# Kernel tuning notes

Measured on AMD Instinct MI355X. Metric: run time of the kernel, lower is better.

Reference implementation:

```python
import jax, jax.numpy as jnp
import numpy as np

V, N, H, A_DIM, F_OUT = 3, 8192, 128, 64, 128


def setup_inputs() -> dict:
    key = jax.random.key(0)
    ks = jax.random.split(key, 13)
    s = 0.02
    w = lambda k, shape: jax.random.normal(k, shape, jnp.float32) * s
    adj = jax.random.randint(ks[0], (V, N, N), 0, 2, dtype=jnp.int32)
    return {
        "adjacency_matrices_list": adj,
        "W1": w(ks[1], (V, N, H)), "b1": w(ks[2], (V, H)),
        "W2": w(ks[3], (V, H, H)), "b2": w(ks[4], (V, H)),
        "Wa1": w(ks[5], (H, A_DIM)), "ba1": w(ks[6], (A_DIM,)),
        "Wa2": w(ks[7], (A_DIM, 1)), "ba2": w(ks[8], (1,)),
        "Wf1": w(ks[9], (H * V, 2 * H)), "bf1": w(ks[10], (2 * H,)),
        "Wf2": w(ks[11], (2 * H, F_OUT)), "bf2": w(ks[12], (F_OUT,)),
    }


def _norm_adj(adj_int):
    # PyG GCNConv gcn_norm on binary edges: add remaining self-loops, then D^-1/2 (A+I) D^-1/2
    a = (adj_int != 0).astype(jnp.float32)            # (V,N,N) binary
    eye = jnp.eye(adj_int.shape[-1], dtype=jnp.float32)
    ah = a * (1.0 - eye) + eye                        # force diagonal to exactly 1
    dinv = jax.lax.rsqrt(ah.sum(-1))                  # deg >= 1, safe
    return ah * dinv[..., :, None] * dinv[..., None, :]


def _forward(adj, W1, b1, W2, b2, Wa1, ba1, Wa2, ba2, Wf1, bf1, Wf2, bf2):
    A = _norm_adj(adj)                                # (V,N,N)
    # initial features X = eye(N), so A @ (X @ W1) == A @ W1
    h = jax.nn.relu(jnp.einsum('vnm,vmh->vnh', A, W1) + b1[:, None, :])
    h = jnp.einsum('vnh,vhk->vnk', h, W2)
    h = jax.nn.relu(jnp.einsum('vnm,vmk->vnk', A, h) + b2[:, None, :])  # (V,N,H) view embeddings
    # attention fusion
    summ = h.mean(axis=1)                             # (V,H) view summaries
    scores = (jnp.tanh(summ @ Wa1 + ba1) @ Wa2 + ba2)[:, 0]
    attn = jax.nn.softmax(scores, axis=0)             # (V,)
    weighted = h * attn[:, None, None]
    fusion_in = jnp.transpose(weighted, (1, 0, 2)).reshape(h.shape[1], -1)  # (N, V*H)
    fused = jax.nn.relu(fusion_in @ Wf1 + bf1) @ Wf2 + bf2                  # (N, F_OUT)
    return fused, attn, h


def reference(adjacency_matrices_list, W1, b1, W2, b2, Wa1, ba1, Wa2, ba2, Wf1, bf1, Wf2, bf2):
    return _forward(adjacency_matrices_list, W1, b1, W2, b2, Wa1, ba1, Wa2, ba2, Wf1, bf1, Wf2, bf2)
```

## Files before the change

kernel.cpp:

```cpp
#include <hip/hip_runtime.h>
#include <hip/hip_bf16.h>

#define VV 3
#define NN 8192
#define HH 128
#define ADIM 64
#define FOUT 128
#define KSPLIT 4

typedef short bf16x8 __attribute__((ext_vector_type(8)));
typedef float f32x4 __attribute__((ext_vector_type(4)));
typedef unsigned char uchar;

__device__ __forceinline__ float bf2f(ushort u) {
    union { unsigned int i; float f; } x; x.i = ((unsigned int)u) << 16; return x.f;
}
__device__ __forceinline__ ushort f2bf(float f) {
    union { float f; unsigned int i; } x; x.f = f;
    unsigned int r = (x.i + 0x7FFFu + ((x.i >> 16) & 1u)) >> 16;
    return (ushort)r;
}
__device__ __forceinline__ void async_cp16(const void* g, void* l) {
    __builtin_amdgcn_global_load_lds(
        (const __attribute__((address_space(1))) void*)g,
        (__attribute__((address_space(3))) void*)l, 16, 0, 0);
}

__global__ void zero_k(float* p, int n) {
    int i = blockIdx.x * blockDim.x + threadIdx.x;
    if (i < n) p[i] = 0.0f;
}

__global__ __launch_bounds__(256) void pack_k(const int* __restrict__ adj,
                                              uchar* __restrict__ abits,
                                              int* __restrict__ deg) {
    __shared__ uint lw[32 * 256];
    const int t = threadIdx.x;
    const int r = t >> 1, half = t & 1;
    const int ks = blockIdx.x, mt = blockIdx.y, z = blockIdx.z;
    const int m0 = mt * 128;
    const int n = m0 + r;
    const long rowoff = ((long)z * NN + n) * NN;
    int cnt = 0;
    for (int kc = 0; kc < 32; kc++) {
        const int colbase = ks * (NN / KSPLIT) + kc * 64 + half * 32;
        uint wbits = 0;
        #pragma unroll
        for (int i = 0; i < 8; i++) {
            const int c0 = colbase + i * 4;
            const int4 v = *(const int4*)(adj + rowoff + c0);
            uint b0 = (v.x != 0 || c0 + 0 == n) ? 1u : 0u;
            uint b1 = (v.y != 0 || c0 + 1 == n) ? 1u : 0u;
            uint b2 = (v.z != 0 || c0 + 2 == n) ? 1u : 0u;
            uint b3 = (v.w != 0 || c0 + 3 == n) ? 1u : 0u;
            wbits |= (b0 | (b1 << 1) | (b2 << 2) | (b3 << 3)) << (i * 4);
        }
        cnt += __popc(wbits);
        lw[kc * 256 + r * 2 + half] = wbits;
    }
    atomicAdd(&deg[z * NN + n], cnt);
    __syncthreads();
    const uint4* src = (const uint4*)lw;
    uint4* dst = (uint4*)(abits + ((((long)z * 64 + mt) * 128 + ks * 32) << 10));
    #pragma unroll
    for (int it = 0; it < 8; it++) dst[it * 256 + t] = src[it * 256 + t];
}

__global__ void dinv_k(const int* __restrict__ deg, float* __restrict__ dinv) {
    int i = blockIdx.x * blockDim.x + threadIdx.x;
    if (i < VV * NN) dinv[i] = rsqrtf((float)deg[i]);
}

template<int INF32>
__global__ void transpose_scale_k(const void* __restrict__ in_, ushort* __restrict__ out,
                                  int R, int C, const float* __restrict__ scale, int scale_z) {
    __shared__ ushort tile[32][33];
    const long zo = (long)blockIdx.z * R * C;
    const int c0 = blockIdx.x * 32, r0 = blockIdx.y * 32;
    const int t = threadIdx.x;
    #pragma unroll
    for (int p = 0; p < 4; p++) {
        int e = p * 256 + t; int row = e >> 5, col = e & 31;
        long idx = zo + (long)(r0 + row) * C + c0 + col;
        float x = INF32 ? ((const float*)in_)[idx] : bf2f(((const ushort*)in_)[idx]);
        if (scale) x *= scale[(long)blockIdx.z * scale_z + r0 + row];
        tile[row][col] = f2bf(x);
    }
    __syncthreads();
    #pragma unroll
    for (int p = 0; p < 4; p++) {
        int e = p * 256 + t; int row = e >> 5, col = e & 31;
        out[zo + (long)(c0 + row) * R + r0 + col] = tile[col][row];
    }
}

__global__ __launch_bounds__(256) void gemm_adj_k(
    const uchar* __restrict__ abits,
    const ushort* __restrict__ Bt,
    float* __restrict__ Cpart)
{
    __shared__ __align__(16) uchar As[1024];
    __shared__ __align__(16) ushort Bs[128 * 64];
    const int tid = threadIdx.x, lane = tid & 63, w = tid >> 6;
    const int wr = w >> 1, wc = w & 1;
    const int ks = blockIdx.x, mt = blockIdx.y, z = blockIdx.z;
    const int m0 = mt * 128;
    const int kbeg = ks * (NN / KSPLIT);
    const uchar* Atile = abits + (((long)z * 64 + mt) * 128 << 10);
    const ushort* Bv = Bt + (long)z * 128 * NN;
    f32x4 acc[4][4] = {};

    int srow[4], slcb[4];
    #pragma unroll
    for (int p = 0; p < 4; p++) {
        int slot = (w * 4 + p) * 64 + lane;
        srow[p] = slot >> 3;
        slcb[p] = (slot & 7) ^ (srow[p] & 7);
    }

    for (int k0 = kbeg; k0 < kbeg + NN / KSPLIT; k0 += 64) {
        if (w == 0)
            async_cp16(Atile + ((long)(k0 >> 6) << 10) + lane * 16, As + lane * 16);
        #pragma unroll
        for (int p = 0; p < 4; p++) {
            const int slot = (w * 4 + p) * 64 + lane;
            async_cp16(Bv + (long)srow[p] * NN + k0 + slcb[p] * 8, Bs + slot * 8);
        }
        __syncthreads();
        const int q = lane >> 4;
        #pragma unroll
        for (int s = 0; s < 2; s++) {
            bf16x8 af[4], bb[4];
            #pragma unroll
            for (int mi = 0; mi < 4; mi++) {
                const int r = wr * 64 + mi * 16 + (lane & 15);
                const uint b = As[r * 8 + s * 4 + q];
                union { uint4 u; bf16x8 v; } cvt;
                cvt.u.x = ((b     ) & 1u) * 0x00003F80u | ((b >> 1) & 1u) * 0x3F800000u;
                cvt.u.y = ((b >> 2) & 1u) * 0x00003F80u | ((b >> 3) & 1u) * 0x3F800000u;
                cvt.u.z = ((b >> 4) & 1u) * 0x00003F80u | ((b >> 5) & 1u) * 0x3F800000u;
                cvt.u.w = ((b >> 6) & 1u) * 0x00003F80u | ((b >> 7) & 1u) * 0x3F800000u;
                af[mi] = cvt.v;
            }
            const int ca = s * 4 + q;
            #pragma unroll
            for (int ni = 0; ni < 4; ni++) {
                int r = wc * 64 + ni * 16 + (lane & 15);
                bb[ni] = *(const bf16x8*)&Bs[r * 64 + ((ca ^ (r & 7)) * 8)];
            }
            #pragma unroll
            for (int mi = 0; mi < 4; mi++)
                #pragma unroll
                for (int ni = 0; ni < 4; ni++)
                    acc[mi][ni] = __builtin_amdgcn_mfma_f32_16x16x32_bf16(af[mi], bb[ni], acc[mi][ni], 0, 0, 0);
        }
        __syncthreads();
    }

    float* C = Cpart + ((long)ks * VV + z) * ((long)NN * HH);
    #pragma unroll
    for (int mi = 0; mi < 4; mi++) {
        int rbase = m0 + wr * 64 + mi * 16 + ((lane >> 4) << 2);
        #pragma unroll
        for (int ni = 0; ni < 4; ni++) {
            int col = wc * 64 + ni * 16 + (lane & 15);
            #pragma unroll
            for (int r = 0; r < 4; r++)
                C[(long)(rbase + r) * HH + col] = acc[mi][ni][r];
        }
    }
}

template<int WRITE_F32>
__global__ __launch_bounds__(256) void reduce_k(const float* __restrict__ P,
                                                const float* __restrict__ dinv,
                                                const float* __restrict__ bias,
                                                ushort* __restrict__ hout,
                                                float* __restrict__ fout) {
    const long e = ((long)blockIdx.x * 256 + threadIdx.x) * 4;
    const int v = (int)(e >> 20);
    const int n = (int)((e >> 7) & (NN - 1));
    const int col = (int)(e & 127);
    const long S = (long)VV * NN * HH;
    const float4 s0 = *(const float4*)(P + e);
    const float4 s1 = *(const float4*)(P + S + e);
    const float4 s2 = *(const float4*)(P + 2 * S + e);
    const float4 s3 = *(const float4*)(P + 3 * S + e);
    const float d = dinv[v * NN + n];
    const float r0 = fmaxf((s0.x + s1.x + s2.x + s3.x) * d + bias[v * HH + col + 0], 0.f);
    const float r1 = fmaxf((s0.y + s1.y + s2.y + s3.y) * d + bias[v * HH + col + 1], 0.f);
    const float r2 = fmaxf((s0.z + s1.z + s2.z + s3.z) * d + bias[v * HH + col + 2], 0.f);
    const float r3 = fmaxf((s0.w + s1.w + s2.w + s3.w) * d + bias[v * HH + col + 3], 0.f);
    ushort4 o; o.x = f2bf(r0); o.y = f2bf(r1); o.z = f2bf(r2); o.w = f2bf(r3);
    *(ushort4*)(hout + e) = o;
    if (WRITE_F32) { float4 f; f.x = r0; f.y = r1; f.z = r2; f.w = r3; *(float4*)(fout + e) = f; }
}

template<int AMODE, int EPI, int OUTF32>
__global__ __launch_bounds__(256) void gemm_k(
    const void* __restrict__ Aany, long a_zs, int lda,
    const ushort* __restrict__ Bt, long b_zs, int ldb,
    void* __restrict__ Cc, long c_zs, int ldc,
    int Ktot,
    const float* __restrict__ dinv, int dinv_zs,
    const float* __restrict__ bias, int bias_zs,
    const float* __restrict__ attnp)
{
    __shared__ __align__(16) ushort As[128][40];
    __shared__ __align__(16) ushort Bs[128][40];
    const int tid = threadIdx.x;
    const int bx = blockIdx.x, by = blockIdx.y, z = blockIdx.z;
    const int m0 = by * 128, n0 = bx * 128;
    const int lane = tid & 63, w = tid >> 6, wr = w >> 1, wc = w & 1;
    f32x4 acc[4][4] = {};
    float att0 = 0.f, att1 = 0.f, att2 = 0.f;
    if (AMODE == 2) { att0 = attnp[0]; att1 = attnp[1]; att2 = attnp[2]; }
    const ushort* Ab = (const ushort*)Aany + (long)z * (AMODE == 1 ? a_zs : 0);
    const ushort* Btz = Bt + (long)z * b_zs;

    for (int k0 = 0; k0 < Ktot; k0 += 32) {
        if (AMODE == 1) {
            #pragma unroll
            for (int p = 0; p < 2; p++) {
                int c = p * 256 + tid;
                int row = c >> 2, q = c & 3;
                *(int4*)&As[row][q * 8] = *(const int4*)(Ab + (long)(m0 + row) * lda + k0 + q * 8);
            }
        } else {
            #pragma unroll
            for (int p = 0; p < 2; p++) {
                int c = p * 256 + tid;
                int row = c >> 2, q = c & 3;
                int kk = k0 + q * 8;
                int v = kk >> 7, ko = kk & 127;
                int4 raw = *(const int4*)((const ushort*)Aany + (long)v * a_zs + (long)(m0 + row) * HH + ko);
                float sc = (v == 0) ? att0 : (v == 1 ? att1 : att2);
                __align__(16) ushort us[8];
                *(int4*)us = raw;
                #pragma unroll
                for (int e = 0; e < 8; e++) us[e] = f2bf(bf2f(us[e]) * sc);
                *(int4*)&As[row][q * 8] = *(int4*)us;
            }
        }
        #pragma unroll
        for (int p = 0; p < 2; p++) {
            int c = p * 256 + tid;
            int n = c >> 2, q = c & 3;
            *(int4*)&Bs[n][q * 8] = *(const int4*)(Btz + (long)(n0 + n) * ldb + k0 + q * 8);
        }
        __syncthreads();
        bf16x8 af[4], bfr[4];
        #pragma unroll
        for (int mi = 0; mi < 4; mi++)
            af[mi] = *(const bf16x8*)&As[wr * 64 + mi * 16 + (lane & 15)][(lane >> 4) * 8];
        #pragma unroll
        for (int ni = 0; ni < 4; ni++)
            bfr[ni] = *(const bf16x8*)&Bs[wc * 64 + ni * 16 + (lane & 15)][(lane >> 4) * 8];
        #pragma unroll
        for (int mi = 0; mi < 4; mi++)
            #pragma unroll
            for (int ni = 0; ni < 4; ni++)
                acc[mi][ni] = __builtin_amdgcn_mfma_f32_16x16x32_bf16(af[mi], bfr[ni], acc[mi][ni], 0, 0, 0);
        __syncthreads();
    }

    #pragma unroll
    for (int mi = 0; mi < 4; mi++) {
        int rbase = m0 + wr * 64 + mi * 16 + ((lane >> 4) << 2);
        #pragma unroll
        for (int ni = 0; ni < 4; ni++) {
            int col = n0 + wc * 64 + ni * 16 + (lane & 15);
            #pragma unroll
            for (int r = 0; r < 4; r++) {
                int grow = rbase + r;
                float vv = acc[mi][ni][r];
                if (EPI == 1) vv *= dinv[(long)z * dinv_zs + grow];
                if (EPI == 2 || EPI == 3) vv += bias[col];
                if (EPI == 2) vv = fmaxf(vv, 0.0f);
                if (OUTF32) ((float*)Cc + (long)z * c_zs)[(long)grow * ldc + col] = vv;
                else        ((ushort*)Cc + (long)z * c_zs)[(long)grow * ldc + col] = f2bf(vv);
            }
        }
    }
}

__global__ __launch_bounds__(256) void colsum_k(const ushort* __restrict__ h2,
                                                float* __restrict__ summ) {
    const int rowbase = blockIdx.x * 64;
    const int z = rowbase >> 13;
    const int col = threadIdx.x & 127, half = threadIdx.x >> 7;
    float s = 0.0f;
    for (int r = half; r < 64; r += 2) s += bf2f(h2[(long)(rowbase + r) * HH + col]);
    atomicAdd(&summ[z * HH + col], s);
}

__global__ __launch_bounds__(256) void attn_k(const float* __restrict__ summ,
                                              const float* __restrict__ Wa1,
                                              const float* __restrict__ ba1,
                                              const float* __restrict__ Wa2,
                                              const float* __restrict__ ba2,
                                              float* __restrict__ attnws,
                                              float* __restrict__ out_attn) {
    __shared__ float sc[VV];
    const int tid = threadIdx.x;
    if (tid < VV * 64) {
        const int v = tid >> 6, a = tid & 63;
        float s = ba1[a];
        const float invN = 1.0f / (float)NN;
        #pragma unroll 4
        for (int h = 0; h < HH; h++) s += summ[v * HH + h] * invN * Wa1[h * ADIM + a];
        float p = tanhf(s) * Wa2[a];
        for (int off = 32; off; off >>= 1) p += __shfl_down(p, off);
        if (a == 0) sc[v] = p + ba2[0];
    }
    __syncthreads();
    if (tid == 0) {
        float m = fmaxf(sc[0], fmaxf(sc[1], sc[2]));
        float e0 = expf(sc[0] - m), e1 = expf(sc[1] - m), e2 = expf(sc[2] - m);
        float inv = 1.0f / (e0 + e1 + e2);
        attnws[0] = e0 * inv; attnws[1] = e1 * inv; attnws[2] = e2 * inv;
        out_attn[0] = e0 * inv; out_attn[1] = e1 * inv; out_attn[2] = e2 * inv;
    }
}

extern "C" void kernel_launch(void* const* d_in, const int* in_sizes, int n_in,
                              void* d_out, int out_size, void* d_ws, size_t ws_size,
                              hipStream_t stream) {
    const int*   adj = (const int*)d_in[0];
    const float* W1  = (const float*)d_in[1];
    const float* b1  = (const float*)d_in[2];
    const float* W2  = (const float*)d_in[3];
    const float* b2  = (const float*)d_in[4];
    const float* Wa1 = (const float*)d_in[5];
    const float* ba1 = (const float*)d_in[6];
    const float* Wa2 = (const float*)d_in[7];
    const float* ba2 = (const float*)d_in[8];
    const float* Wf1 = (const float*)d_in[9];
    const float* bf1 = (const float*)d_in[10];
    const float* Wf2 = (const float*)d_in[11];
    const float* bf2v = (const float*)d_in[12];

    float* out = (float*)d_out;
    float* out_fused = out;
    float* out_attn  = out + (long)NN * FOUT;
    float* out_h     = out + (long)NN * FOUT + VV;

    char* wsb = (char*)d_ws;
    const long SZ_DINV  = (long)VV * NN * 4;
    const long SZ_ABITS = (long)VV * 64 * 128 * 1024;
    const long SZ_W1T   = (long)VV * HH * NN * 2;
    const long SZ_W2T   = (long)VV * HH * HH * 2;
    const long SZ_WF1T  = 256L * 384 * 2;
    const long SZ_WF2T  = 128L * 256 * 2;
    const long SZ_VNH   = (long)VV * NN * HH * 2;
    const long SZ_PART  = (long)KSPLIT * VV * NN * HH * 4;
    const long SZ_G     = (long)NN * 256 * 2;
    long off = 0;
    float*  dinv  = (float*)(wsb + off);  off += SZ_DINV;
    uchar*  abits = (uchar*)(wsb + off);  off += SZ_ABITS;
    ushort* w1t   = (ushort*)(wsb + off); off += SZ_W1T;
    ushort* w2t   = (ushort*)(wsb + off); off += SZ_W2T;
    ushort* wf1t  = (ushort*)(wsb + off); off += SZ_WF1T;
    ushort* wf2t  = (ushort*)(wsb + off); off += SZ_WF2T;
    ushort* h1    = (ushort*)(wsb + off); off += SZ_VNH;
    ushort* tbuf  = (ushort*)(wsb + off); off += SZ_VNH;
    ushort* tT    = (ushort*)(wsb + off); off += SZ_VNH;
    ushort* h2    = (ushort*)(wsb + off); off += SZ_VNH;
    float*  cpart = (float*)(wsb + off);  off += SZ_PART;
    ushort* G     = (ushort*)(wsb + off); off += SZ_G;
    float*  summ  = (float*)(wsb + off);  off += 1600;
    float*  attnw = summ + 384;
    int*    deg   = (int*)(wsb + off);    off += (long)VV * NN * 4;

    const long VNH = (long)NN * HH;

    zero_k<<<98, 256, 0, stream>>>(summ, 400 + VV * NN);
    pack_k<<<dim3(KSPLIT, 64, VV), 256, 0, stream>>>(adj, abits, deg);
    dinv_k<<<96, 256, 0, stream>>>(deg, dinv);
    transpose_scale_k<1><<<dim3(4, 256, VV), 256, 0, stream>>>(W1, w1t, NN, HH, dinv, NN);
    transpose_scale_k<1><<<dim3(4, 4, VV), 256, 0, stream>>>(W2, w2t, HH, HH, nullptr, 0);
    transpose_scale_k<1><<<dim3(8, 12, 1), 256, 0, stream>>>(Wf1, wf1t, 384, 256, nullptr, 0);
    transpose_scale_k<1><<<dim3(4, 8, 1), 256, 0, stream>>>(Wf2, wf2t, 256, 128, nullptr, 0);
    gemm_adj_k<<<dim3(KSPLIT, 64, VV), 256, 0, stream>>>(abits, w1t, cpart);
    reduce_k<0><<<3072, 256, 0, stream>>>(cpart, dinv, b1, h1, nullptr);
    gemm_k<1, 1, 0><<<dim3(1, 64, VV), 256, 0, stream>>>(h1, VNH, HH, w2t, (long)HH * HH, HH,
                                                         tbuf, VNH, HH, HH, dinv, NN, nullptr, 0, nullptr);
    transpose_scale_k<0><<<dim3(4, 256, VV), 256, 0, stream>>>(tbuf, tT, NN, HH, nullptr, 0);
    gemm_adj_k<<<dim3(KSPLIT, 64, VV), 256, 0, stream>>>(abits, tT, cpart);
    reduce_k<1><<<3072, 256, 0, stream>>>(cpart, dinv, b2, h2, out_h);
    colsum_k<<<(VV * NN) / 64, 256, 0, stream>>>(h2, summ);
    attn_k<<<1, 256, 0, stream>>>(summ, Wa1, ba1, Wa2, ba2, attnw, out_attn);
    gemm_k<2, 2, 0><<<dim3(2, 64, 1), 256, 0, stream>>>(h2, VNH, HH, wf1t, 0, 384,
                                                        G, 0, 256, 384, nullptr, 0, bf1, 0, attnw);
    gemm_k<1, 3, 1><<<dim3(1, 64, 1), 256, 0, stream>>>(G, 0, 256, wf2t, 0, 256,
                                                        out_fused, 0, FOUT, 256, nullptr, 0, bf2v, 0, nullptr);
}
```

Measured before the change: 1.500 ms.

## Drop split-K in adjacency GEMM and fuse normalization epilogue and degree computation

Removes the KSPLIT=4 partitioning of the adjacency GEMM so that each block runs the full K loop. The scale, bias and ReLU epilogue is done in-register instead of through fp32 partial buffers and a separate reduce kernel. The pack kernel now walks full rows and computes dinv directly with a lane shuffle, which removes the atomics, the degree buffer and the dinv kernel. This cuts partial-sum traffic and several launches. In exchange, parallelism drops sharply: the pack kernel goes to 192 blocks and the GEMM to 384 blocks of 2 waves, which risks underfilling the GPU and exposing memory latency.

```diff
diff --git a/kernel.cpp b/kernel.cpp
--- a/kernel.cpp
+++ b/kernel.cpp
@@ -6,7 +6,6 @@
 #define HH 128
 #define ADIM 64
 #define FOUT 128
-#define KSPLIT 4
 
 typedef short bf16x8 __attribute__((ext_vector_type(8)));
 typedef float f32x4 __attribute__((ext_vector_type(4)));
@@ -33,17 +32,16 @@
 
 __global__ __launch_bounds__(256) void pack_k(const int* __restrict__ adj,
                                               uchar* __restrict__ abits,
-                                              int* __restrict__ deg) {
-    __shared__ uint lw[32 * 256];
+                                              float* __restrict__ dinv) {
     const int t = threadIdx.x;
     const int r = t >> 1, half = t & 1;
-    const int ks = blockIdx.x, mt = blockIdx.y, z = blockIdx.z;
-    const int m0 = mt * 128;
-    const int n = m0 + r;
+    const int mt = blockIdx.x, z = blockIdx.y;
+    const int n = mt * 128 + r;
     const long rowoff = ((long)z * NN + n) * NN;
+    uint* dst = (uint*)(abits + (((long)z * 64 + mt) * 128 << 10));
     int cnt = 0;
-    for (int kc = 0; kc < 32; kc++) {
-        const int colbase = ks * (NN / KSPLIT) + kc * 64 + half * 32;
+    for (int kc = 0; kc < 128; kc++) {
+        const int colbase = kc * 64 + half * 32;
         uint wbits = 0;
         #pragma unroll
         for (int i = 0; i < 8; i++) {
@@ -56,19 +54,10 @@
             wbits |= (b0 | (b1 << 1) | (b2 << 2) | (b3 << 3)) << (i * 4);
         }
         cnt += __popc(wbits);
-        lw[kc * 256 + r * 2 + half] = wbits;
-    }
-    atomicAdd(&deg[z * NN + n], cnt);
-    __syncthreads();
-    const uint4* src = (const uint4*)lw;
-    uint4* dst = (uint4*)(abits + ((((long)z * 64 + mt) * 128 + ks * 32) << 10));
-    #pragma unroll
-    for (int it = 0; it < 8; it++) dst[it * 256 + t] = src[it * 256 + t];
-}
-
-__global__ void dinv_k(const int* __restrict__ deg, float* __restrict__ dinv) {
-    int i = blockIdx.x * blockDim.x + threadIdx.x;
-    if (i < VV * NN) dinv[i] = rsqrtf((float)deg[i]);
+        dst[kc * 256 + t] = wbits;
+    }
+    cnt += __shfl_xor(cnt, 1);
+    if (half == 0) dinv[(long)z * NN + n] = rsqrtf((float)cnt);
 }
 
 template<int INF32>
@@ -94,106 +83,91 @@
     }
 }
 
-__global__ __launch_bounds__(256) void gemm_adj_k(
+template<int WRITE_F32>
+__global__ __launch_bounds__(128) void gemm_adj_k(
     const uchar* __restrict__ abits,
     const ushort* __restrict__ Bt,
-    float* __restrict__ Cpart)
+    const float* __restrict__ dinv,
+    const float* __restrict__ bias,
+    ushort* __restrict__ hout,
+    float* __restrict__ fout)
 {
-    __shared__ __align__(16) uchar As[1024];
+    __shared__ __align__(16) uchar As[512];
     __shared__ __align__(16) ushort Bs[128 * 64];
-    const int tid = threadIdx.x, lane = tid & 63, w = tid >> 6;
-    const int wr = w >> 1, wc = w & 1;
-    const int ks = blockIdx.x, mt = blockIdx.y, z = blockIdx.z;
-    const int m0 = mt * 128;
-    const int kbeg = ks * (NN / KSPLIT);
-    const uchar* Atile = abits + (((long)z * 64 + mt) * 128 << 10);
+    const int tid = threadIdx.x, lane = tid & 63, wc = tid >> 6;
+    const int mt = blockIdx.x, z = blockIdx.y;
+    const int m0 = mt * 64;
+    const uchar* Achunks = abits + (((long)z * 64 + (mt >> 1)) * 128 << 10);
+    const int arow_off = (mt & 1) * 512;
     const ushort* Bv = Bt + (long)z * 128 * NN;
     f32x4 acc[4][4] = {};
 
-    int srow[4], slcb[4];
-    #pragma unroll
-    for (int p = 0; p < 4; p++) {
-        int slot = (w * 4 + p) * 64 + lane;
+    int srow[8], slcb[8];
+    #pragma unroll
+    for (int p = 0; p < 8; p++) {
+        int slot = p * 128 + tid;
         srow[p] = slot >> 3;
         slcb[p] = (slot & 7) ^ (srow[p] & 7);
     }
 
-    for (int k0 = kbeg; k0 < kbeg + NN / KSPLIT; k0 += 64) {
-        if (w == 0)
-            async_cp16(Atile + ((long)(k0 >> 6) << 10) + lane * 16, As + lane * 16);
-        #pragma unroll
-        for (int p = 0; p < 4; p++) {
-            const int slot = (w * 4 + p) * 64 + lane;
+    for (int kc = 0; kc < 128; kc++) {
+        if (tid < 32)
+            async_cp16(Achunks + ((long)kc << 10) + arow_off + tid * 16, As + tid * 16);
+        const int k0 = kc * 64;
+        #pragma unroll
+        for (int p = 0; p < 8; p++) {
+            const int slot = p * 128 + tid;
             async_cp16(Bv + (long)srow[p] * NN + k0 + slcb[p] * 8, Bs + slot * 8);
         }
         __syncthreads();
         const int q = lane >> 4;
+        uint2 bitsarr[4];
+        #pragma unroll
+        for (int mi = 0; mi < 4; mi++)
+            bitsarr[mi] = *(const uint2*)&As[(mi * 16 + (lane & 15)) * 8];
         #pragma unroll
         for (int s = 0; s < 2; s++) {
-            bf16x8 af[4], bb[4];
+            bf16x8 bb[4];
+            const int ca = s * 4 + q;
+            #pragma unroll
+            for (int ni = 0; ni < 4; ni++) {
+                int r = wc * 64 + ni * 16 + (lane & 15);
+                bb[ni] = *(const bf16x8*)&Bs[r * 64 + ((ca ^ (r & 7)) * 8)];
+            }
             #pragma unroll
             for (int mi = 0; mi < 4; mi++) {
-                const int r = wr * 64 + mi * 16 + (lane & 15);
-                const uint b = As[r * 8 + s * 4 + q];
+                const uint wsel = s ? bitsarr[mi].y : bitsarr[mi].x;
+                const uint b = (wsel >> (q * 8)) & 0xffu;
                 union { uint4 u; bf16x8 v; } cvt;
                 cvt.u.x = ((b     ) & 1u) * 0x00003F80u | ((b >> 1) & 1u) * 0x3F800000u;
                 cvt.u.y = ((b >> 2) & 1u) * 0x00003F80u | ((b >> 3) & 1u) * 0x3F800000u;
                 cvt.u.z = ((b >> 4) & 1u) * 0x00003F80u | ((b >> 5) & 1u) * 0x3F800000u;
                 cvt.u.w = ((b >> 6) & 1u) * 0x00003F80u | ((b >> 7) & 1u) * 0x3F800000u;
-                af[mi] = cvt.v;
-            }
-            const int ca = s * 4 + q;
-            #pragma unroll
-            for (int ni = 0; ni < 4; ni++) {
-                int r = wc * 64 + ni * 16 + (lane & 15);
-                bb[ni] = *(const bf16x8*)&Bs[r * 64 + ((ca ^ (r & 7)) * 8)];
-            }
-            #pragma unroll
-            for (int mi = 0; mi < 4; mi++)
                 #pragma unroll
                 for (int ni = 0; ni < 4; ni++)
-                    acc[mi][ni] = __builtin_amdgcn_mfma_f32_16x16x32_bf16(af[mi], bb[ni], acc[mi][ni], 0, 0, 0);
+                    acc[mi][ni] = __builtin_amdgcn_mfma_f32_16x16x32_bf16(cvt.v, bb[ni], acc[mi][ni], 0, 0, 0);
+            }
         }
         __syncthreads();
     }
 
-    float* C = Cpart + ((long)ks * VV + z) * ((long)NN * HH);
+    const long zo = (long)z * NN * HH;
     #pragma unroll
     for (int mi = 0; mi < 4; mi++) {
-        int rbase = m0 + wr * 64 + mi * 16 + ((lane >> 4) << 2);
+        int rbase = m0 + mi * 16 + ((lane >> 4) << 2);
         #pragma unroll
         for (int ni = 0; ni < 4; ni++) {
             int col = wc * 64 + ni * 16 + (lane & 15);
-            #pragma unroll
-            for (int r = 0; r < 4; r++)
-                C[(long)(rbase + r) * HH + col] = acc[mi][ni][r];
-        }
-    }
-}
-
-template<int WRITE_F32>
-__global__ __launch_bounds__(256) void reduce_k(const float* __restrict__ P,
-                                                const float* __restrict__ dinv,
-                                                const float* __restrict__ bias,
-                                                ushort* __restrict__ hout,
-                                                float* __restrict__ fout) {
-    const long e = ((long)blockIdx.x * 256 + threadIdx.x) * 4;
-    const int v = (int)(e >> 20);
-    const int n = (int)((e >> 7) & (NN - 1));
-    const int col = (int)(e & 127);
-    const long S = (long)VV * NN * HH;
-    const float4 s0 = *(const float4*)(P + e);
-    const float4 s1 = *(const float4*)(P + S + e);
-    const float4 s2 = *(const float4*)(P + 2 * S + e);
-    const float4 s3 = *(const float4*)(P + 3 * S + e);
-    const float d = dinv[v * NN + n];
-    const float r0 = fmaxf((s0.x + s1.x + s2.x + s3.x) * d + bias[v * HH + col + 0], 0.f);
-    const float r1 = fmaxf((s0.y + s1.y + s2.y + s3.y) * d + bias[v * HH + col + 1], 0.f);
-    const float r2 = fmaxf((s0.z + s1.z + s2.z + s3.z) * d + bias[v * HH + col + 2], 0.f);
-    const float r3 = fmaxf((s0.w + s1.w + s2.w + s3.w) * d + bias[v * HH + col + 3], 0.f);
-    ushort4 o; o.x = f2bf(r0); o.y = f2bf(r1); o.z = f2bf(r2); o.w = f2bf(r3);
-    *(ushort4*)(hout + e) = o;
-    if (WRITE_F32) { float4 f; f.x = r0; f.y = r1; f.z = r2; f.w = r3; *(float4*)(fout + e) = f; }
+            float bcol = bias[z * HH + col];
+            #pragma unroll
+            for (int r = 0; r < 4; r++) {
+                int grow = rbase + r;
+                float v = fmaxf(acc[mi][ni][r] * dinv[(long)z * NN + grow] + bcol, 0.0f);
+                hout[zo + (long)grow * HH + col] = f2bf(v);
+                if (WRITE_F32) fout[zo + (long)grow * HH + col] = v;
+            }
+        }
+    }
 }
 
 template<int AMODE, int EPI, int OUTF32>
@@ -211,7 +185,7 @@
     const int tid = threadIdx.x;
     const int bx = blockIdx.x, by = blockIdx.y, z = blockIdx.z;
     const int m0 = by * 128, n0 = bx * 128;
-    const int lane = tid & 63, w = tid >> 6, wr = w >> 1, wc = w & 1;
+    const int lane = tid & 63, w = tid >> 6, wr = w >> 1, wcq = w & 1;
     f32x4 acc[4][4] = {};
     float att0 = 0.f, att1 = 0.f, att2 = 0.f;
     if (AMODE == 2) { att0 = attnp[0]; att1 = attnp[1]; att2 = attnp[2]; }
@@ -255,7 +229,7 @@
             af[mi] = *(const bf16x8*)&As[wr * 64 + mi * 16 + (lane & 15)][(lane >> 4) * 8];
         #pragma unroll
         for (int ni = 0; ni < 4; ni++)
-            bfr[ni] = *(const bf16x8*)&Bs[wc * 64 + ni * 16 + (lane & 15)][(lane >> 4) * 8];
+            bfr[ni] = *(const bf16x8*)&Bs[wcq * 64 + ni * 16 + (lane & 15)][(lane >> 4) * 8];
         #pragma unroll
         for (int mi = 0; mi < 4; mi++)
             #pragma unroll
@@ -269,7 +243,7 @@
         int rbase = m0 + wr * 64 + mi * 16 + ((lane >> 4) << 2);
         #pragma unroll
         for (int ni = 0; ni < 4; ni++) {
-            int col = n0 + wc * 64 + ni * 16 + (lane & 15);
+            int col = n0 + wcq * 64 + ni * 16 + (lane & 15);
             #pragma unroll
             for (int r = 0; r < 4; r++) {
                 int grow = rbase + r;
@@ -353,7 +327,6 @@
     const long SZ_WF1T  = 256L * 384 * 2;
     const long SZ_WF2T  = 128L * 256 * 2;
     const long SZ_VNH   = (long)VV * NN * HH * 2;
-    const long SZ_PART  = (long)KSPLIT * VV * NN * HH * 4;
     const long SZ_G     = (long)NN * 256 * 2;
     long off = 0;
     float*  dinv  = (float*)(wsb + off);  off += SZ_DINV;
@@ -366,28 +339,23 @@
     ushort* tbuf  = (ushort*)(wsb + off); off += SZ_VNH;
     ushort* tT    = (ushort*)(wsb + off); off += SZ_VNH;
     ushort* h2    = (ushort*)(wsb + off); off += SZ_VNH;
-    float*  cpart = (float*)(wsb + off);  off += SZ_PART;
     ushort* G     = (ushort*)(wsb + off); off += SZ_G;
     float*  summ  = (float*)(wsb + off);  off += 1600;
     float*  attnw = summ + 384;
-    int*    deg   = (int*)(wsb + off);    off += (long)VV * NN * 4;
 
     const long VNH = (long)NN * HH;
 
-    zero_k<<<98, 256, 0, stream>>>(summ, 400 + VV * NN);
-    pack_k<<<dim3(KSPLIT, 64, VV), 256, 0, stream>>>(adj, abits, deg);
-    dinv_k<<<96, 256, 0, stream>>>(deg, dinv);
+    zero_k<<<2, 256, 0, stream>>>(summ, 400);
+    pack_k<<<dim3(64, VV), 256, 0, stream>>>(adj, abits, dinv);
     transpose_scale_k<1><<<dim3(4, 256, VV), 256, 0, stream>>>(W1, w1t, NN, HH, dinv, NN);
     transpose_scale_k<1><<<dim3(4, 4, VV), 256, 0, stream>>>(W2, w2t, HH, HH, nullptr, 0);
     transpose_scale_k<1><<<dim3(8, 12, 1), 256, 0, stream>>>(Wf1, wf1t, 384, 256, nullptr, 0);
     transpose_scale_k<1><<<dim3(4, 8, 1), 256, 0, stream>>>(Wf2, wf2t, 256, 128, nullptr, 0);
-    gemm_adj_k<<<dim3(KSPLIT, 64, VV), 256, 0, stream>>>(abits, w1t, cpart);
-    reduce_k<0><<<3072, 256, 0, stream>>>(cpart, dinv, b1, h1, nullptr);
+    gemm_adj_k<0><<<dim3(128, VV), 128, 0, stream>>>(abits, w1t, dinv, b1, h1, nullptr);
     gemm_k<1, 1, 0><<<dim3(1, 64, VV), 256, 0, stream>>>(h1, VNH, HH, w2t, (long)HH * HH, HH,
                                                          tbuf, VNH, HH, HH, dinv, NN, nullptr, 0, nullptr);
     transpose_scale_k<0><<<dim3(4, 256, VV), 256, 0, stream>>>(tbuf, tT, NN, HH, nullptr, 0);
-    gemm_adj_k<<<dim3(KSPLIT, 64, VV), 256, 0, stream>>>(abits, tT, cpart);
-    reduce_k<1><<<3072, 256, 0, stream>>>(cpart, dinv, b2, h2, out_h);
+    gemm_adj_k<1><<<dim3(128, VV), 128, 0, stream>>>(abits, tT, dinv, b2, h2, out_h);
     colsum_k<<<(VV * NN) / 64, 256, 0, stream>>>(h2, summ);
     attn_k<<<1, 256, 0, stream>>>(summ, Wa1, ba1, Wa2, ba2, attnw, out_attn);
     gemm_k<2, 2, 0><<<dim3(2, 64, 1), 256, 0, stream>>>(h2, VNH, HH, wf1t, 0, 384,
```

Result: slower. 1.542 ms (+2.8%).

## Restructure adjacency packing to one wave per row with fused degree

Applied to the files above, without the earlier changes.

The adjacency bit-packing kernel now assigns one wavefront to each full row. Lanes read contiguous int4 chunks, so each wave's loads are fully coalesced, where before two threads strode through each row. Bits are assembled with wave shuffles, and the row degree comes from a wave reduction that writes dinv directly. This removes the atomic degree accumulation, the separate dinv kernel and most of the zeroing kernel. The cost is more shuffle work and narrower 8-byte strided stores into the tiled bit layout.

```diff
diff --git a/kernel.cpp b/kernel.cpp
--- a/kernel.cpp
+++ b/kernel.cpp
@@ -33,42 +33,40 @@
 
 __global__ __launch_bounds__(256) void pack_k(const int* __restrict__ adj,
                                               uchar* __restrict__ abits,
-                                              int* __restrict__ deg) {
-    __shared__ uint lw[32 * 256];
-    const int t = threadIdx.x;
-    const int r = t >> 1, half = t & 1;
-    const int ks = blockIdx.x, mt = blockIdx.y, z = blockIdx.z;
-    const int m0 = mt * 128;
-    const int n = m0 + r;
-    const long rowoff = ((long)z * NN + n) * NN;
+                                              float* __restrict__ dinv) {
+    __shared__ uint rowbuf[4][256];
+    const int t = threadIdx.x, w = t >> 6, lane = t & 63;
+    const long rowg = (long)blockIdx.x * 4 + w;
+    const int n = (int)(rowg & (NN - 1));
+    const int z = (int)(rowg >> 13);
+    const int mt = n >> 7, r = n & 127;
+    const int* row = adj + rowg * NN;
     int cnt = 0;
-    for (int kc = 0; kc < 32; kc++) {
-        const int colbase = ks * (NN / KSPLIT) + kc * 64 + half * 32;
-        uint wbits = 0;
-        #pragma unroll
-        for (int i = 0; i < 8; i++) {
-            const int c0 = colbase + i * 4;
-            const int4 v = *(const int4*)(adj + rowoff + c0);
-            uint b0 = (v.x != 0 || c0 + 0 == n) ? 1u : 0u;
-            uint b1 = (v.y != 0 || c0 + 1 == n) ? 1u : 0u;
-            uint b2 = (v.z != 0 || c0 + 2 == n) ? 1u : 0u;
-            uint b3 = (v.w != 0 || c0 + 3 == n) ? 1u : 0u;
-            wbits |= (b0 | (b1 << 1) | (b2 << 2) | (b3 << 3)) << (i * 4);
-        }
-        cnt += __popc(wbits);
-        lw[kc * 256 + r * 2 + half] = wbits;
-    }
-    atomicAdd(&deg[z * NN + n], cnt);
+    for (int it = 0; it < 32; it++) {
+        const int c0 = it * 256 + lane * 4;
+        const int4 v = *(const int4*)(row + c0);
+        uint nib = (uint)(v.x != 0 || c0 + 0 == n)
+                 | ((uint)(v.y != 0 || c0 + 1 == n) << 1)
+                 | ((uint)(v.z != 0 || c0 + 2 == n) << 2)
+                 | ((uint)(v.w != 0 || c0 + 3 == n) << 3);
+        cnt += __popc(nib);
+        uint x = nib << ((lane & 1) * 4);
+        x |= __shfl_xor(x, 1);
+        x <<= ((lane >> 1) & 1) * 8;
+        x |= __shfl_xor(x, 2);
+        x <<= ((lane >> 2) & 1) * 16;
+        x |= __shfl_xor(x, 4);
+        if ((lane & 7) == 0) rowbuf[w][it * 8 + (lane >> 3)] = x;
+    }
+    for (int off = 32; off; off >>= 1) cnt += __shfl_down(cnt, off);
+    if (lane == 0) dinv[rowg] = rsqrtf((float)cnt);
     __syncthreads();
-    const uint4* src = (const uint4*)lw;
-    uint4* dst = (uint4*)(abits + ((((long)z * 64 + mt) * 128 + ks * 32) << 10));
-    #pragma unroll
-    for (int it = 0; it < 8; it++) dst[it * 256 + t] = src[it * 256 + t];
-}
-
-__global__ void dinv_k(const int* __restrict__ deg, float* __restrict__ dinv) {
-    int i = blockIdx.x * blockDim.x + threadIdx.x;
-    if (i < VV * NN) dinv[i] = rsqrtf((float)deg[i]);
+    uint2* dstbase = (uint2*)(abits + (((long)z * 64 + mt) * 128 << 10) + r * 8);
+    #pragma unroll
+    for (int ph = 0; ph < 2; ph++) {
+        const int kc = ph * 64 + lane;
+        dstbase[(long)kc * 128] = *(const uint2*)&rowbuf[w][kc * 2];
+    }
 }
 
 template<int INF32>
@@ -145,8 +143,8 @@
             const int ca = s * 4 + q;
             #pragma unroll
             for (int ni = 0; ni < 4; ni++) {
-                int r = wc * 64 + ni * 16 + (lane & 15);
-                bb[ni] = *(const bf16x8*)&Bs[r * 64 + ((ca ^ (r & 7)) * 8)];
+                int rr = wc * 64 + ni * 16 + (lane & 15);
+                bb[ni] = *(const bf16x8*)&Bs[rr * 64 + ((ca ^ (rr & 7)) * 8)];
             }
             #pragma unroll
             for (int mi = 0; mi < 4; mi++)
@@ -211,7 +209,7 @@
     const int tid = threadIdx.x;
     const int bx = blockIdx.x, by = blockIdx.y, z = blockIdx.z;
     const int m0 = by * 128, n0 = bx * 128;
-    const int lane = tid & 63, w = tid >> 6, wr = w >> 1, wc = w & 1;
+    const int lane = tid & 63, w = tid >> 6, wr = w >> 1, wcq = w & 1;
     f32x4 acc[4][4] = {};
     float att0 = 0.f, att1 = 0.f, att2 = 0.f;
     if (AMODE == 2) { att0 = attnp[0]; att1 = attnp[1]; att2 = attnp[2]; }
@@ -255,7 +253,7 @@
             af[mi] = *(const bf16x8*)&As[wr * 64 + mi * 16 + (lane & 15)][(lane >> 4) * 8];
         #pragma unroll
         for (int ni = 0; ni < 4; ni++)
-            bfr[ni] = *(const bf16x8*)&Bs[wc * 64 + ni * 16 + (lane & 15)][(lane >> 4) * 8];
+            bfr[ni] = *(const bf16x8*)&Bs[wcq * 64 + ni * 16 + (lane & 15)][(lane >> 4) * 8];
         #pragma unroll
         for (int mi = 0; mi < 4; mi++)
             #pragma unroll
@@ -269,7 +267,7 @@
         int rbase = m0 + wr * 64 + mi * 16 + ((lane >> 4) << 2);
         #pragma unroll
         for (int ni = 0; ni < 4; ni++) {
-            int col = n0 + wc * 64 + ni * 16 + (lane & 15);
+            int col = n0 + wcq * 64 + ni * 16 + (lane & 15);
             #pragma unroll
             for (int r = 0; r < 4; r++) {
                 int grow = rbase + r;
@@ -370,13 +368,11 @@
     ushort* G     = (ushort*)(wsb + off); off += SZ_G;
     float*  summ  = (float*)(wsb + off);  off += 1600;
     float*  attnw = summ + 384;
-    int*    deg   = (int*)(wsb + off);    off += (long)VV * NN * 4;
 
     const long VNH = (long)NN * HH;
 
-    zero_k<<<98, 256, 0, stream>>>(summ, 400 + VV * NN);
-    pack_k<<<dim3(KSPLIT, 64, VV), 256, 0, stream>>>(adj, abits, deg);
-    dinv_k<<<96, 256, 0, stream>>>(deg, dinv);
+    zero_k<<<2, 256, 0, stream>>>(summ, 400);
+    pack_k<<<(VV * NN) / 4, 256, 0, stream>>>(adj, abits, dinv);
     transpose_scale_k<1><<<dim3(4, 256, VV), 256, 0, stream>>>(W1, w1t, NN, HH, dinv, NN);
     transpose_scale_k<1><<<dim3(4, 4, VV), 256, 0, stream>>>(W2, w2t, HH, HH, nullptr, 0);
     transpose_scale_k<1><<<dim3(8, 12, 1), 256, 0, stream>>>(Wf1, wf1t, 384, 256, nullptr, 0);
```

Result: faster. 1.267 ms (-15.6%).
